# Optimization experiments

Measured on AMD Instinct MI355X. Metric: run time of the kernel, lower is better.

Reference implementation:

```python
import jax, jax.numpy as jnp
import numpy as np

B, CQ, CVK, L, H = 4, 256, 256, 2048, 8
D = CVK // H  # depth per head = 32
EPS = 1e-5    # BatchNorm eps


def setup_inputs() -> dict:
    key = jax.random.key(0)
    ks = jax.random.split(key, 32)
    n = lambda i, s, sc=1.0: jax.random.normal(ks[i], s, dtype=jnp.float32) * sc
    u = lambda i, s: jax.random.uniform(ks[i], s, dtype=jnp.float32, minval=0.5, maxval=1.5)
    inp = {
        'v': n(0, (B, CVK, L)), 'k': n(1, (B, CVK, L)), 'q': n(2, (B, CQ, L)),
        # trainable positional encodings (pe_q: image_shape_q, pe_vk: image_shape_vk)
        'pe_q': n(3, (CQ, L)), 'pe_vk': n(4, (CVK, L)),
        # W_query / W_key / W_value: Conv1d(kernel=1) weight [out,in] + bias, then BatchNorm1d (eval mode)
        'wq': n(5, (CVK, CQ), 0.05), 'bq': n(6, (CVK,), 0.05),
        'gq': 1.0 + n(7, (CVK,), 0.1), 'betaq': n(8, (CVK,), 0.1), 'mq': n(9, (CVK,), 0.1), 'varq': u(10, (CVK,)),
        'wk': n(11, (CVK, CVK), 0.05), 'bk': n(12, (CVK,), 0.05),
        'gk': 1.0 + n(13, (CVK,), 0.1), 'betak': n(14, (CVK,), 0.1), 'mk': n(15, (CVK,), 0.1), 'vark': u(16, (CVK,)),
        'wv': n(17, (CVK, CVK), 0.05), 'bv': n(18, (CVK,), 0.05),
        'gv': 1.0 + n(19, (CVK,), 0.1), 'betav': n(20, (CVK,), 0.1), 'mv': n(21, (CVK,), 0.1), 'varv': u(22, (CVK,)),
        # out_proj (zero-init in original; randomized here so gradients are non-trivial)
        'wo': n(23, (CQ, CVK), 0.05), 'bo': n(24, (CQ,), 0.05),
    }
    return inp


def _conv1(x, w, b):  # 1x1 conv == channel matmul: [b,c,l] -> [b,o,l]
    return jnp.einsum('oc,bcl->bol', w, x) + b[None, :, None]


def _bn(x, g, beta, mean, var):  # eval-mode BatchNorm1d over channel dim
    scale = g / jnp.sqrt(var + EPS)
    return (x - mean[:, None]) * scale[:, None] + beta[:, None]


def _mha(v, k, q, pe_q, pe_vk, wq, bq, gq, betaq, mq, varq,
         wk, bk, gk, betak, mk, vark, wv, bv, gv, betav, mv, varv, wo, bo):
    q_orig = q
    b = q.shape[0]
    vv = v + pe_vk[None]
    kk = k + pe_vk[None]
    qq = q + pe_q[None]
    qp = _bn(_conv1(qq, wq, bq), gq, betaq, mq, varq)   # [b, CVK, L]
    kp = _bn(_conv1(kk, wk, bk), gk, betak, mk, vark)
    vp = _bn(_conv1(vv, wv, bv), gv, betav, mv, varv)
    # split heads: [b, H, D, L]
    qh = qp.reshape(b, H, D, -1)
    kh = kp.reshape(b, H, D, -1)
    vh = vp.reshape(b, H, D, -1)
    # scaled dot-product attention over sequence dim (l: query pos, m: key pos)
    scores = jnp.einsum('bhdl,bhdm->bhlm', qh, kh) / jnp.sqrt(jnp.float32(D))
    p = jax.nn.softmax(scores, axis=-1)
    a = jnp.einsum('bhlm,bhdm->bhdl', p, vh)            # [b, H, D, L]
    a = a.reshape(b, H * D, -1)                          # [b, CVK, L]
    out = _conv1(a, wo, bo)                              # [b, CQ, L]
    return q_orig + out


def reference(v, k, q, pe_q, pe_vk, wq, bq, gq, betaq, mq, varq,
              wk, bk, gk, betak, mk, vark, wv, bv, gv, betav, mv, varv, wo, bo):
    return _mha(v, k, q, pe_q, pe_vk, wq, bq, gq, betaq, mq, varq,
                wk, bk, gk, betak, mk, vark, wv, bv, gv, betav, mv, varv, wo, bo)
```

## Files before the change

kernel.cpp:

```cpp
#include <hip/hip_runtime.h>
#include <hip/hip_bf16.h>

#define BB 4
#define CC 256
#define LL 2048
#define HH 8
#define DD 32
#define EPSV 1e-5f

typedef __bf16 bf16x8 __attribute__((ext_vector_type(8)));
typedef __bf16 bf16x4 __attribute__((ext_vector_type(4)));
typedef __bf16 bf16x2 __attribute__((ext_vector_type(2)));
typedef float  f32x4  __attribute__((ext_vector_type(4)));
typedef float  f32x16 __attribute__((ext_vector_type(16)));
typedef unsigned int u32x4 __attribute__((ext_vector_type(4)));

static __device__ __forceinline__ unsigned pkbf(float lo, float hi) {
    bf16x2 p; p[0] = (__bf16)lo; p[1] = (__bf16)hi;
    return __builtin_bit_cast(unsigned, p);
}

__global__ __launch_bounds__(512) void qkv_gemm_kernel(
    const float* __restrict__ qin, const float* __restrict__ kin,
    const float* __restrict__ vin,
    const float* __restrict__ peq, const float* __restrict__ pevk,
    const float* __restrict__ wq, const float* __restrict__ bq,
    const float* __restrict__ gq, const float* __restrict__ betaq,
    const float* __restrict__ mq, const float* __restrict__ varq,
    const float* __restrict__ wk, const float* __restrict__ bk,
    const float* __restrict__ gk, const float* __restrict__ betak,
    const float* __restrict__ mk, const float* __restrict__ vark,
    const float* __restrict__ wv, const float* __restrict__ bv,
    const float* __restrict__ gv, const float* __restrict__ betav,
    const float* __restrict__ mv, const float* __restrict__ varv,
    __bf16* __restrict__ qTo, __bf16* __restrict__ kTo, __bf16* __restrict__ vNo,
    float qscale)
{
    __shared__ __align__(16) __bf16 Wl[64][136];
    __shared__ __align__(16) __bf16 Xl[128][136];
    __bf16 (*Tl)[72] = (__bf16(*)[72])Xl;

    const int z = blockIdx.z;
    const int which = z >> 2;
    const int b = z & 3;
    const float* X    = which==0 ? qin : (which==1 ? kin : vin);
    const float* pe   = which==0 ? peq : pevk;
    const float* W    = which==0 ? wq  : (which==1 ? wk  : wv);
    const float* bia  = which==0 ? bq  : (which==1 ? bk  : bv);
    const float* gam  = which==0 ? gq  : (which==1 ? gk  : gv);
    const float* bet  = which==0 ? betaq : (which==1 ? betak : betav);
    const float* mea  = which==0 ? mq  : (which==1 ? mk  : mv);
    const float* var  = which==0 ? varq : (which==1 ? vark : varv);
    const float extra = (which==0) ? qscale : 1.0f;

    const int lt = blockIdx.x * 128;
    const int ot = blockIdx.y * 64;
    const int t  = threadIdx.x;
    const int wvi = t >> 6;
    const int wm = wvi >> 2;
    const int wn = wvi & 3;
    const int l  = t & 63;
    const int lq = l & 15;
    const int g  = l >> 4;

    f32x4 acc[2][2];
    #pragma unroll
    for (int mi = 0; mi < 2; ++mi)
        #pragma unroll
        for (int ni = 0; ni < 2; ++ni) acc[mi][ni] = (f32x4){0.f,0.f,0.f,0.f};

    for (int ks = 0; ks < 2; ++ks) {
        __syncthreads();
        #pragma unroll
        for (int i = 0; i < 4; ++i) {
            const int idx = i * 512 + t;
            const int row = idx >> 5;
            const int ch  = idx & 31;
            const int o   = ot + row;
            const float sc = gam[o] * rsqrtf(var[o] + EPSV) * extra;
            const float4 w4 = *(const float4*)&W[(size_t)o * CC + ks * 128 + ch * 4];
            bf16x4 wb;
            wb[0] = (__bf16)(w4.x * sc); wb[1] = (__bf16)(w4.y * sc);
            wb[2] = (__bf16)(w4.z * sc); wb[3] = (__bf16)(w4.w * sc);
            *(bf16x4*)&Wl[row][ch * 4] = wb;
        }
        #pragma unroll
        for (int i = 0; i < 2; ++i) {
            const int slot = i * 512 + t;
            const int lp = slot & 63;
            const int co = slot >> 6;
            const float* xp = &X[(size_t)(b * CC + ks * 128 + co * 8) * LL + lt + lp * 2];
            const float* pp = &pe[(size_t)(ks * 128 + co * 8) * LL + lt + lp * 2];
            bf16x8 lo, hi;
            #pragma unroll
            for (int j = 0; j < 8; ++j) {
                const float2 a = *(const float2*)&xp[(size_t)j * LL];
                const float2 p = *(const float2*)&pp[(size_t)j * LL];
                lo[j] = (__bf16)(a.x + p.x);
                hi[j] = (__bf16)(a.y + p.y);
            }
            *(bf16x8*)&Xl[lp * 2    ][co * 8] = lo;
            *(bf16x8*)&Xl[lp * 2 + 1][co * 8] = hi;
        }
        __syncthreads();

        #pragma unroll
        for (int kk = 0; kk < 4; ++kk) {
            bf16x8 af[2], bfr[2];
            #pragma unroll
            for (int mi = 0; mi < 2; ++mi)
                af[mi] = *(const bf16x8*)&Wl[wm * 32 + mi * 16 + lq][kk * 32 + g * 8];
            #pragma unroll
            for (int ni = 0; ni < 2; ++ni)
                bfr[ni] = *(const bf16x8*)&Xl[wn * 32 + ni * 16 + lq][kk * 32 + g * 8];
            #pragma unroll
            for (int mi = 0; mi < 2; ++mi)
                #pragma unroll
                for (int ni = 0; ni < 2; ++ni)
                    acc[mi][ni] = __builtin_amdgcn_mfma_f32_16x16x32_bf16(
                        af[mi], bfr[ni], acc[mi][ni], 0, 0, 0);
        }
    }

    float bb[2][4];
    #pragma unroll
    for (int mi = 0; mi < 2; ++mi) {
        const int o4 = ot + wm * 32 + mi * 16 + g * 4;
        const float4 b4 = *(const float4*)&bia[o4];
        const float4 g4 = *(const float4*)&gam[o4];
        const float4 v4 = *(const float4*)&var[o4];
        const float4 m4 = *(const float4*)&mea[o4];
        const float4 t4 = *(const float4*)&bet[o4];
        const float bs[4] = {b4.x,b4.y,b4.z,b4.w};
        const float gs[4] = {g4.x,g4.y,g4.z,g4.w};
        const float vs[4] = {v4.x,v4.y,v4.z,v4.w};
        const float ms[4] = {m4.x,m4.y,m4.z,m4.w};
        const float ts[4] = {t4.x,t4.y,t4.z,t4.w};
        #pragma unroll
        for (int r = 0; r < 4; ++r) {
            const float sc = gs[r] * rsqrtf(vs[r] + EPSV);
            bb[mi][r] = ((bs[r] - ms[r]) * sc + ts[r]) * extra;
        }
    }

    if (which < 2) {
        __bf16* outT = which==0 ? qTo : kTo;
        __syncthreads();
        #pragma unroll
        for (int mi = 0; mi < 2; ++mi) {
            #pragma unroll
            for (int ni = 0; ni < 2; ++ni) {
                bf16x4 pv;
                #pragma unroll
                for (int r = 0; r < 4; ++r) pv[r] = (__bf16)(acc[mi][ni][r] + bb[mi][r]);
                *(bf16x4*)&Tl[wn * 32 + ni * 16 + lq][wm * 32 + mi * 16 + g * 4] = pv;
            }
        }
        __syncthreads();
        #pragma unroll
        for (int i = 0; i < 2; ++i) {
            const int idx = i * 512 + t;
            const int lrow = idx >> 3, ch = idx & 7;
            *(bf16x8*)&outT[(size_t)(b * LL + lt + lrow) * CC + ot + ch * 8] =
                *(const bf16x8*)&Tl[lrow][ch * 8];
        }
    } else {
        #pragma unroll
        for (int mi = 0; mi < 2; ++mi) {
            #pragma unroll
            for (int ni = 0; ni < 2; ++ni) {
                const int col = lt + wn * 32 + ni * 16 + lq;
                #pragma unroll
                for (int r = 0; r < 4; ++r) {
                    const int o = ot + wm * 32 + mi * 16 + g * 4 + r;
                    vNo[(size_t)(b * CC + o) * LL + col] = (__bf16)(acc[mi][ni][r] + bb[mi][r]);
                }
            }
        }
    }
}

__global__ __launch_bounds__(256, 2) void attn_mfma_kernel(
    const __bf16* __restrict__ qT, const __bf16* __restrict__ kT,
    const __bf16* __restrict__ vN, __bf16* __restrict__ aT)
{
    __shared__ __align__(16) __bf16 KB[2][128 * 32];
    __shared__ __align__(16) __bf16 VB[2][32 * 128];

    const int flat = blockIdx.x + 16 * (blockIdx.y + 8 * blockIdx.z);
    const int xcd  = flat & 7;
    const int ixc  = flat >> 3;
    const int gidx = xcd + 8 * (ixc >> 4);
    const int qb   = ixc & 15;
    const int h    = gidx & 7;
    const int b    = gidx >> 3;

    const int t  = threadIdx.x;
    const int w  = t >> 6;
    const int l  = t & 63;
    const int lq = l & 31;
    const int hi = l >> 5;

    const int q0 = qb * 128 + w * 32;

    const __bf16* qrow = qT + ((size_t)(b * LL) + q0 + lq) * CC + h * DD;
    const bf16x8 qf0 = *(const bf16x8*)&qrow[hi * 8];
    const bf16x8 qf1 = *(const bf16x8*)&qrow[16 + hi * 8];

    const __bf16* kTb = kT + (size_t)(b * LL) * CC + h * DD;
    const __bf16* vNb = vN + ((size_t)(b * CC) + h * DD) * LL;

    const int s0 = t, s1 = 256 + t;
    const int sk0 = s0 >> 2, sp0 = s0 & 3;
    const int sk1 = s1 >> 2, sp1 = s1 & 3;
    const int sd0 = s0 >> 4, sv0 = s0 & 15;
    const int sd1 = s1 >> 4, sv1 = s1 & 15;
    const int kw0 = sk0 * 32 + (sp0 ^ ((sk0 >> 1) & 3)) * 8;
    const int kw1 = sk1 * 32 + (sp1 ^ ((sk1 >> 1) & 3)) * 8;
    const int vw0 = sd0 * 128 + (sv0 ^ (sd0 & 7)) * 8;
    const int vw1 = sd1 * 128 + (sv1 ^ (sd1 & 7)) * 8;

    bf16x8 kr0, kr1, vr0, vr1;
    #define LOADREGS(KT0) \
        kr0 = *(const bf16x8*)&kTb[(size_t)((KT0) + sk0) * CC + sp0 * 8]; \
        kr1 = *(const bf16x8*)&kTb[(size_t)((KT0) + sk1) * CC + sp1 * 8]; \
        vr0 = *(const bf16x8*)&vNb[(size_t)sd0 * LL + (KT0) + sv0 * 8];   \
        vr1 = *(const bf16x8*)&vNb[(size_t)sd1 * LL + (KT0) + sv1 * 8];
    #define WRITEBUF(BUF) \
        *(bf16x8*)&KB[BUF][kw0] = kr0; *(bf16x8*)&KB[BUF][kw1] = kr1; \
        *(bf16x8*)&VB[BUF][vw0] = vr0; *(bf16x8*)&VB[BUF][vw1] = vr1;

    LOADREGS(0)
    WRITEBUF(0)
    LOADREGS(128)

    f32x16 O;
    #pragma unroll
    for (int r = 0; r < 16; ++r) O[r] = 0.f;
    float ssum = 0.f;
    f32x16 Z16;
    #pragma unroll
    for (int r = 0; r < 16; ++r) Z16[r] = 0.f;

    #define QKC(kbv, S) { \
        const int key_ = (kbv) + lq; \
        const int ksw_ = (key_ >> 1) & 3; \
        const bf16x8 kf0_ = *(const bf16x8*)&KBb[key_ * 32 + ((hi    ) ^ ksw_) * 8]; \
        const bf16x8 kf1_ = *(const bf16x8*)&KBb[key_ * 32 + ((2 + hi) ^ ksw_) * 8]; \
        S = __builtin_amdgcn_mfma_f32_32x32x16_bf16(kf0_, qf0, Z16, 0, 0, 0); \
        S = __builtin_amdgcn_mfma_f32_32x32x16_bf16(kf1_, qf1, S, 0, 0, 0); }

    #define SMC(S, P0, P1) { \
        float e_[16]; \
        _Pragma("unroll") \
        for (int r = 0; r < 16; ++r) e_[r] = __builtin_amdgcn_exp2f(S[r]); \
        float s_ = 0.f; \
        _Pragma("unroll") \
        for (int r = 0; r < 16; r += 4) s_ += (e_[r] + e_[r+1]) + (e_[r+2] + e_[r+3]); \
        ssum += s_; \
        unsigned a_[8]; \
        _Pragma("unroll") \
        for (int i = 0; i < 8; ++i) a_[i] = pkbf(e_[2*i], e_[2*i+1]); \
        { unsigned w0_ = a_[0], w1_ = a_[1], w2_ = a_[2], w3_ = a_[3]; \
          asm volatile("v_permlane32_swap_b32 %0, %1" : "+v"(w0_), "+v"(w2_)); \
          asm volatile("v_permlane32_swap_b32 %0, %1" : "+v"(w1_), "+v"(w3_)); \
          P0 = (u32x4){w0_, w1_, w2_, w3_}; } \
        { unsigned w0_ = a_[4], w1_ = a_[5], w2_ = a_[6], w3_ = a_[7]; \
          asm volatile("v_permlane32_swap_b32 %0, %1" : "+v"(w0_), "+v"(w2_)); \
          asm volatile("v_permlane32_swap_b32 %0, %1" : "+v"(w1_), "+v"(w3_)); \
          P1 = (u32x4){w0_, w1_, w2_, w3_}; } }

    #define PVC(kbv, P0, P1) { \
        const bf16x8 pf0_ = __builtin_bit_cast(bf16x8, P0); \
        const bf16x8 vf0_ = *(const bf16x8*)&VBb[lq * 128 + ((((kbv) >> 3) + hi    ) ^ (lq & 7)) * 8]; \
        O = __builtin_amdgcn_mfma_f32_32x32x16_bf16(vf0_, pf0_, O, 0, 0, 0); \
        const bf16x8 pf1_ = __builtin_bit_cast(bf16x8, P1); \
        const bf16x8 vf1_ = *(const bf16x8*)&VBb[lq * 128 + ((((kbv) >> 3) + 2 + hi) ^ (lq & 7)) * 8]; \
        O = __builtin_amdgcn_mfma_f32_32x32x16_bf16(vf1_, pf1_, O, 0, 0, 0); }

    const int NT = LL / 128;
    for (int it = 0; it < NT; ++it) {
        const int buf = it & 1;
        __syncthreads();
        if (it + 1 < NT) { WRITEBUF(buf ^ 1) }
        if (it + 2 < NT) { LOADREGS((it + 2) * 128) }

        const __bf16* KBb = KB[buf];
        const __bf16* VBb = VB[buf];

        f32x16 S0, S1, S2, S3;
        u32x4 P0a, P0b, P1a, P1b, P2a, P2b, P3a, P3b;
        QKC(0,  S0)
        QKC(32, S1)
        SMC(S0, P0a, P0b)
        QKC(64, S2)
        PVC(0,  P0a, P0b)
        SMC(S1, P1a, P1b)
        QKC(96, S3)
        PVC(32, P1a, P1b)
        SMC(S2, P2a, P2b)
        PVC(64, P2a, P2b)
        SMC(S3, P3a, P3b)
        PVC(96, P3a, P3b)
    }
    #undef LOADREGS
    #undef WRITEBUF
    #undef QKC
    #undef SMC
    #undef PVC

    ssum += __shfl_xor(ssum, 32);
    const float inv = 1.f / ssum;

    __bf16* arow = aT + ((size_t)(b * LL) + q0 + lq) * CC + h * DD;
    #pragma unroll
    for (int gi = 0; gi < 4; ++gi) {
        bf16x4 ov;
        #pragma unroll
        for (int r = 0; r < 4; ++r) ov[r] = (__bf16)(O[4*gi + r] * inv);
        *(bf16x4*)&arow[8 * gi + 4 * hi] = ov;
    }
}

__global__ __launch_bounds__(256) void outproj_kernel(
    const float* __restrict__ W, const __bf16* __restrict__ X,
    const float* __restrict__ bias, const float* __restrict__ resid,
    float* __restrict__ outF)
{
    __shared__ __align__(16) __bf16 Wl[64][136];
    __shared__ __align__(16) __bf16 Xl[64][136];

    const int lt = blockIdx.x * 64;
    const int ot = blockIdx.y * 64;
    const int b  = blockIdx.z;
    const int t  = threadIdx.x;
    const int wvi = t >> 6;
    const int wm = wvi >> 1;
    const int wn = wvi & 1;
    const int l  = t & 63;
    const int lq = l & 15;
    const int g  = l >> 4;

    f32x4 acc[2][2];
    #pragma unroll
    for (int mi = 0; mi < 2; ++mi)
        #pragma unroll
        for (int ni = 0; ni < 2; ++ni) acc[mi][ni] = (f32x4){0.f,0.f,0.f,0.f};

    for (int ks = 0; ks < 2; ++ks) {
        __syncthreads();
        #pragma unroll
        for (int i = 0; i < 8; ++i) {
            const int idx = i * 256 + t;
            const int row = idx >> 5;
            const int ch  = idx & 31;
            const float4 w4 = *(const float4*)&W[(size_t)(ot + row) * CC + ks * 128 + ch * 4];
            bf16x4 wb;
            wb[0] = (__bf16)w4.x; wb[1] = (__bf16)w4.y;
            wb[2] = (__bf16)w4.z; wb[3] = (__bf16)w4.w;
            *(bf16x4*)&Wl[row][ch * 4] = wb;
        }
        #pragma unroll
        for (int i = 0; i < 4; ++i) {
            const int idx = i * 256 + t;
            const int row = idx >> 4, ch = idx & 15;
            *(bf16x8*)&Xl[row][ch * 8] =
                *(const bf16x8*)&X[(size_t)(b * LL + lt + row) * CC + ks * 128 + ch * 8];
        }
        __syncthreads();

        #pragma unroll
        for (int kk = 0; kk < 4; ++kk) {
            bf16x8 af[2], bfr[2];
            #pragma unroll
            for (int mi = 0; mi < 2; ++mi)
                af[mi] = *(const bf16x8*)&Wl[wm * 32 + mi * 16 + lq][kk * 32 + g * 8];
            #pragma unroll
            for (int ni = 0; ni < 2; ++ni)
                bfr[ni] = *(const bf16x8*)&Xl[wn * 32 + ni * 16 + lq][kk * 32 + g * 8];
            #pragma unroll
            for (int mi = 0; mi < 2; ++mi)
                #pragma unroll
                for (int ni = 0; ni < 2; ++ni)
                    acc[mi][ni] = __builtin_amdgcn_mfma_f32_16x16x32_bf16(
                        af[mi], bfr[ni], acc[mi][ni], 0, 0, 0);
        }
    }

    #pragma unroll
    for (int mi = 0; mi < 2; ++mi) {
        const float4 b4 = *(const float4*)&bias[ot + wm * 32 + mi * 16 + g * 4];
        const float bb[4] = {b4.x, b4.y, b4.z, b4.w};
        #pragma unroll
        for (int ni = 0; ni < 2; ++ni) {
            const int col = lt + wn * 32 + ni * 16 + lq;
            #pragma unroll
            for (int r = 0; r < 4; ++r) {
                const int o = ot + wm * 32 + mi * 16 + g * 4 + r;
                const size_t a = (size_t)(b * CC + o) * LL + col;
                outF[a] = acc[mi][ni][r] + bb[r] + resid[a];
            }
        }
    }
}

extern "C" void kernel_launch(void* const* d_in, const int* in_sizes, int n_in,
                              void* d_out, int out_size, void* d_ws, size_t ws_size,
                              hipStream_t stream)
{
    const float* v     = (const float*)d_in[0];
    const float* k     = (const float*)d_in[1];
    const float* q     = (const float*)d_in[2];
    const float* pe_q  = (const float*)d_in[3];
    const float* pe_vk = (const float*)d_in[4];
    const float* wq    = (const float*)d_in[5];
    const float* bq    = (const float*)d_in[6];
    const float* gq    = (const float*)d_in[7];
    const float* betaq = (const float*)d_in[8];
    const float* mq    = (const float*)d_in[9];
    const float* varq  = (const float*)d_in[10];
    const float* wk    = (const float*)d_in[11];
    const float* bk    = (const float*)d_in[12];
    const float* gk    = (const float*)d_in[13];
    const float* betak = (const float*)d_in[14];
    const float* mk    = (const float*)d_in[15];
    const float* vark  = (const float*)d_in[16];
    const float* wv    = (const float*)d_in[17];
    const float* bv    = (const float*)d_in[18];
    const float* gv    = (const float*)d_in[19];
    const float* betav = (const float*)d_in[20];
    const float* mv    = (const float*)d_in[21];
    const float* varv  = (const float*)d_in[22];
    const float* wo    = (const float*)d_in[23];
    const float* bo    = (const float*)d_in[24];

    float* out = (float*)d_out;

    const size_t E = (size_t)BB * CC * LL;
    __bf16* qT  = (__bf16*)d_ws;
    __bf16* kT  = qT + E;
    __bf16* vN  = kT + E;
    __bf16* aT  = vN + E;

    const float qscale = 0.17677669529663687f * 1.4426950408889634f;

    hipLaunchKernelGGL(qkv_gemm_kernel, dim3(16, 4, 12), dim3(512), 0, stream,
                       q, k, v, pe_q, pe_vk,
                       wq, bq, gq, betaq, mq, varq,
                       wk, bk, gk, betak, mk, vark,
                       wv, bv, gv, betav, mv, varv,
                       qT, kT, vN, qscale);

    hipLaunchKernelGGL(attn_mfma_kernel, dim3(16, HH, BB), dim3(256), 0, stream,
                       qT, kT, vN, aT);

    hipLaunchKernelGGL(outproj_kernel, dim3(32, 4, 4), dim3(256), 0, stream,
                       wo, aT, bo, q, out);
}
```

Measured before the change: 60.53 us.

## Split attention key range in two halves and add combine kernel

Attention blocks now each process half of the key sequence (split-K), doubling the grid from 512 to 1024 blocks. Each block writes unnormalized fp32 partial outputs and row sums to workspace, and a new combine kernel adds the two halves, normalizes and writes the bf16 attention output. The softmax has no running max, so the partials can simply be summed. The QK/PV schedule is also reordered to use fewer score registers, and the occupancy hint is dropped. This adds an extra launch and fp32 partial traffic (strided, uncoalesced-ish writes) in exchange for more parallelism.

```diff
diff --git a/kernel.cpp b/kernel.cpp
--- a/kernel.cpp
+++ b/kernel.cpp
@@ -180,20 +180,23 @@
     }
 }
 
-__global__ __launch_bounds__(256, 2) void attn_mfma_kernel(
+__global__ __launch_bounds__(256) void attn_mfma_kernel(
     const __bf16* __restrict__ qT, const __bf16* __restrict__ kT,
-    const __bf16* __restrict__ vN, __bf16* __restrict__ aT)
+    const __bf16* __restrict__ vN, float* __restrict__ Ow,
+    float* __restrict__ Sw)
 {
     __shared__ __align__(16) __bf16 KB[2][128 * 32];
     __shared__ __align__(16) __bf16 VB[2][32 * 128];
 
-    const int flat = blockIdx.x + 16 * (blockIdx.y + 8 * blockIdx.z);
+    const int flat = blockIdx.x + 16 * (blockIdx.y + 16 * blockIdx.z);
     const int xcd  = flat & 7;
     const int ixc  = flat >> 3;
     const int gidx = xcd + 8 * (ixc >> 4);
     const int qb   = ixc & 15;
-    const int h    = gidx & 7;
-    const int b    = gidx >> 3;
+    const int b    = gidx >> 4;
+    const int y    = gidx & 15;
+    const int h    = y >> 1;
+    const int half = y & 1;
 
     const int t  = threadIdx.x;
     const int w  = t >> 6;
@@ -202,6 +205,7 @@
     const int hi = l >> 5;
 
     const int q0 = qb * 128 + w * 32;
+    const int kbase = half * 1024;
 
     const __bf16* qrow = qT + ((size_t)(b * LL) + q0 + lq) * CC + h * DD;
     const bf16x8 qf0 = *(const bf16x8*)&qrow[hi * 8];
@@ -230,9 +234,9 @@
         *(bf16x8*)&KB[BUF][kw0] = kr0; *(bf16x8*)&KB[BUF][kw1] = kr1; \
         *(bf16x8*)&VB[BUF][vw0] = vr0; *(bf16x8*)&VB[BUF][vw1] = vr1;
 
-    LOADREGS(0)
+    LOADREGS(kbase)
     WRITEBUF(0)
-    LOADREGS(128)
+    LOADREGS(kbase + 128)
 
     f32x16 O;
     #pragma unroll
@@ -278,30 +282,30 @@
         const bf16x8 vf1_ = *(const bf16x8*)&VBb[lq * 128 + ((((kbv) >> 3) + 2 + hi) ^ (lq & 7)) * 8]; \
         O = __builtin_amdgcn_mfma_f32_32x32x16_bf16(vf1_, pf1_, O, 0, 0, 0); }
 
-    const int NT = LL / 128;
+    const int NT = 1024 / 128;
     for (int it = 0; it < NT; ++it) {
         const int buf = it & 1;
         __syncthreads();
         if (it + 1 < NT) { WRITEBUF(buf ^ 1) }
-        if (it + 2 < NT) { LOADREGS((it + 2) * 128) }
+        if (it + 2 < NT) { LOADREGS(kbase + (it + 2) * 128) }
 
         const __bf16* KBb = KB[buf];
         const __bf16* VBb = VB[buf];
 
-        f32x16 S0, S1, S2, S3;
-        u32x4 P0a, P0b, P1a, P1b, P2a, P2b, P3a, P3b;
+        f32x16 S0, S1;
+        u32x4 Pa, Pb;
         QKC(0,  S0)
         QKC(32, S1)
-        SMC(S0, P0a, P0b)
-        QKC(64, S2)
-        PVC(0,  P0a, P0b)
-        SMC(S1, P1a, P1b)
-        QKC(96, S3)
-        PVC(32, P1a, P1b)
-        SMC(S2, P2a, P2b)
-        PVC(64, P2a, P2b)
-        SMC(S3, P3a, P3b)
-        PVC(96, P3a, P3b)
+        SMC(S0, Pa, Pb)
+        PVC(0,  Pa, Pb)
+        QKC(64, S0)
+        SMC(S1, Pa, Pb)
+        PVC(32, Pa, Pb)
+        QKC(96, S1)
+        SMC(S0, Pa, Pb)
+        PVC(64, Pa, Pb)
+        SMC(S1, Pa, Pb)
+        PVC(96, Pa, Pb)
     }
     #undef LOADREGS
     #undef WRITEBUF
@@ -310,16 +314,53 @@
     #undef PVC
 
     ssum += __shfl_xor(ssum, 32);
-    const float inv = 1.f / ssum;
-
-    __bf16* arow = aT + ((size_t)(b * LL) + q0 + lq) * CC + h * DD;
+
+    float* orow = Ow + (size_t)(((b * HH + h) * 2 + half) * DD) * LL;
     #pragma unroll
     for (int gi = 0; gi < 4; ++gi) {
-        bf16x4 ov;
-        #pragma unroll
-        for (int r = 0; r < 4; ++r) ov[r] = (__bf16)(O[4*gi + r] * inv);
-        *(bf16x4*)&arow[8 * gi + 4 * hi] = ov;
-    }
+        #pragma unroll
+        for (int r = 0; r < 4; ++r) {
+            const int d = 8 * gi + 4 * hi + r;
+            orow[(size_t)d * LL + q0 + lq] = O[4 * gi + r];
+        }
+    }
+    if (l < 32)
+        Sw[(size_t)((b * HH + h) * 2 + half) * LL + q0 + lq] = ssum;
+}
+
+__global__ __launch_bounds__(256) void combine_kernel(
+    const float* __restrict__ Ow, const float* __restrict__ Sw,
+    __bf16* __restrict__ aT)
+{
+    __shared__ float invs[64];
+    __shared__ __align__(16) __bf16 Tl[64][40];
+
+    const int lt = blockIdx.x * 64;
+    const int h  = blockIdx.y;
+    const int b  = blockIdx.z;
+    const int t  = threadIdx.x;
+
+    if (t < 64) {
+        const float s0 = Sw[(size_t)((b * HH + h) * 2 + 0) * LL + lt + t];
+        const float s1 = Sw[(size_t)((b * HH + h) * 2 + 1) * LL + lt + t];
+        invs[t] = 1.f / (s0 + s1);
+    }
+    __syncthreads();
+
+    const float* O0 = Ow + (size_t)(((b * HH + h) * 2 + 0) * DD) * LL;
+    const float* O1 = Ow + (size_t)(((b * HH + h) * 2 + 1) * DD) * LL;
+    #pragma unroll
+    for (int i = 0; i < 8; ++i) {
+        const int idx = i * 256 + t;
+        const int d = idx >> 6, q = idx & 63;
+        const float v = (O0[(size_t)d * LL + lt + q] + O1[(size_t)d * LL + lt + q]) * invs[q];
+        Tl[q][d] = (__bf16)v;
+    }
+    __syncthreads();
+
+    const int q = t >> 2, dc = t & 3;
+    *(bf16x8*)&aT[((size_t)(b * LL) + lt + q) * CC + h * DD + dc * 8] =
+        *(const bf16x8*)&Tl[q][dc * 8];
 }
 
 __global__ __launch_bounds__(256) void outproj_kernel(
@@ -441,6 +482,8 @@
     __bf16* kT  = qT + E;
     __bf16* vN  = kT + E;
     __bf16* aT  = vN + E;
+    float*  Ow  = (float*)(aT + E);
+    float*  Sw  = Ow + 2 * E;
 
     const float qscale = 0.17677669529663687f * 1.4426950408889634f;
 
@@ -451,8 +494,11 @@
                        wv, bv, gv, betav, mv, varv,
                        qT, kT, vN, qscale);
 
-    hipLaunchKernelGGL(attn_mfma_kernel, dim3(16, HH, BB), dim3(256), 0, stream,
-                       qT, kT, vN, aT);
+    hipLaunchKernelGGL(attn_mfma_kernel, dim3(16, 16, BB), dim3(256), 0, stream,
+                       qT, kT, vN, Ow, Sw);
+
+    hipLaunchKernelGGL(combine_kernel, dim3(32, HH, BB), dim3(256), 0, stream,
+                       Ow, Sw, aT);
 
     hipLaunchKernelGGL(outproj_kernel, dim3(32, 4, 4), dim3(256), 0, stream,
                        wo, aT, bo, q, out);
```

Result: slower. 70.50 us (+16.5%).

## Split attention key range across two wave groups per block and merge via LDS

Applied to the files above, without the earlier changes.

The attention block doubles to 512 threads. Two halves each process half of the key sequence (1024 keys) with their own double-buffered K/V LDS tiles, and the partial O and row sums are combined through shared memory at the end. This is meant to raise parallelism and latency hiding given only 512 blocks on the GPU. The inner loop also reuses fewer S/P registers to reduce pressure. The merge only adds the partial sums with no max rescaling, so it is correct only if the softmax is computed without a running max. The extra LDS, barriers and combine step add cost.

```diff
diff --git a/kernel.cpp b/kernel.cpp
--- a/kernel.cpp
+++ b/kernel.cpp
@@ -180,12 +180,12 @@
     }
 }
 
-__global__ __launch_bounds__(256, 2) void attn_mfma_kernel(
+__global__ __launch_bounds__(512) void attn_mfma_kernel(
     const __bf16* __restrict__ qT, const __bf16* __restrict__ kT,
     const __bf16* __restrict__ vN, __bf16* __restrict__ aT)
 {
-    __shared__ __align__(16) __bf16 KB[2][128 * 32];
-    __shared__ __align__(16) __bf16 VB[2][32 * 128];
+    __shared__ __align__(16) __bf16 KB[2][2][4096];
+    __shared__ __align__(16) __bf16 VB[2][2][4096];
 
     const int flat = blockIdx.x + 16 * (blockIdx.y + 8 * blockIdx.z);
     const int xcd  = flat & 7;
@@ -197,11 +197,14 @@
 
     const int t  = threadIdx.x;
     const int w  = t >> 6;
+    const int hs = w >> 2;
+    const int wl = w & 3;
     const int l  = t & 63;
     const int lq = l & 31;
     const int hi = l >> 5;
 
-    const int q0 = qb * 128 + w * 32;
+    const int q0 = qb * 128 + wl * 32;
+    const int kbase = hs * 1024;
 
     const __bf16* qrow = qT + ((size_t)(b * LL) + q0 + lq) * CC + h * DD;
     const bf16x8 qf0 = *(const bf16x8*)&qrow[hi * 8];
@@ -210,7 +213,8 @@
     const __bf16* kTb = kT + (size_t)(b * LL) * CC + h * DD;
     const __bf16* vNb = vN + ((size_t)(b * CC) + h * DD) * LL;
 
-    const int s0 = t, s1 = 256 + t;
+    const int th = t & 255;
+    const int s0 = th, s1 = 256 + th;
     const int sk0 = s0 >> 2, sp0 = s0 & 3;
     const int sk1 = s1 >> 2, sp1 = s1 & 3;
     const int sd0 = s0 >> 4, sv0 = s0 & 15;
@@ -220,6 +224,9 @@
     const int vw0 = sd0 * 128 + (sv0 ^ (sd0 & 7)) * 8;
     const int vw1 = sd1 * 128 + (sv1 ^ (sd1 & 7)) * 8;
 
+    __bf16* KBw = &KB[hs][0][0];
+    __bf16* VBw = &VB[hs][0][0];
+
     bf16x8 kr0, kr1, vr0, vr1;
     #define LOADREGS(KT0) \
         kr0 = *(const bf16x8*)&kTb[(size_t)((KT0) + sk0) * CC + sp0 * 8]; \
@@ -227,12 +234,14 @@
         vr0 = *(const bf16x8*)&vNb[(size_t)sd0 * LL + (KT0) + sv0 * 8];   \
         vr1 = *(const bf16x8*)&vNb[(size_t)sd1 * LL + (KT0) + sv1 * 8];
     #define WRITEBUF(BUF) \
-        *(bf16x8*)&KB[BUF][kw0] = kr0; *(bf16x8*)&KB[BUF][kw1] = kr1; \
-        *(bf16x8*)&VB[BUF][vw0] = vr0; *(bf16x8*)&VB[BUF][vw1] = vr1;
-
-    LOADREGS(0)
+        *(bf16x8*)&KBw[(BUF) * 4096 + kw0] = kr0; \
+        *(bf16x8*)&KBw[(BUF) * 4096 + kw1] = kr1; \
+        *(bf16x8*)&VBw[(BUF) * 4096 + vw0] = vr0; \
+        *(bf16x8*)&VBw[(BUF) * 4096 + vw1] = vr1;
+
+    LOADREGS(kbase)
     WRITEBUF(0)
-    LOADREGS(128)
+    LOADREGS(kbase + 128)
 
     f32x16 O;
     #pragma unroll
@@ -278,30 +287,30 @@
         const bf16x8 vf1_ = *(const bf16x8*)&VBb[lq * 128 + ((((kbv) >> 3) + 2 + hi) ^ (lq & 7)) * 8]; \
         O = __builtin_amdgcn_mfma_f32_32x32x16_bf16(vf1_, pf1_, O, 0, 0, 0); }
 
-    const int NT = LL / 128;
+    const int NT = 1024 / 128;
     for (int it = 0; it < NT; ++it) {
         const int buf = it & 1;
         __syncthreads();
         if (it + 1 < NT) { WRITEBUF(buf ^ 1) }
-        if (it + 2 < NT) { LOADREGS((it + 2) * 128) }
-
-        const __bf16* KBb = KB[buf];
-        const __bf16* VBb = VB[buf];
-
-        f32x16 S0, S1, S2, S3;
-        u32x4 P0a, P0b, P1a, P1b, P2a, P2b, P3a, P3b;
+        if (it + 2 < NT) { LOADREGS(kbase + (it + 2) * 128) }
+
+        const __bf16* KBb = &KBw[buf * 4096];
+        const __bf16* VBb = &VBw[buf * 4096];
+
+        f32x16 S0, S1;
+        u32x4 Pa, Pb;
         QKC(0,  S0)
         QKC(32, S1)
-        SMC(S0, P0a, P0b)
-        QKC(64, S2)
-        PVC(0,  P0a, P0b)
-        SMC(S1, P1a, P1b)
-        QKC(96, S3)
-        PVC(32, P1a, P1b)
-        SMC(S2, P2a, P2b)
-        PVC(64, P2a, P2b)
-        SMC(S3, P3a, P3b)
-        PVC(96, P3a, P3b)
+        SMC(S0, Pa, Pb)
+        PVC(0,  Pa, Pb)
+        QKC(64, S0)
+        SMC(S1, Pa, Pb)
+        PVC(32, Pa, Pb)
+        QKC(96, S1)
+        SMC(S0, Pa, Pb)
+        PVC(64, Pa, Pb)
+        SMC(S1, Pa, Pb)
+        PVC(96, Pa, Pb)
     }
     #undef LOADREGS
     #undef WRITEBUF
@@ -310,15 +319,32 @@
     #undef PVC
 
     ssum += __shfl_xor(ssum, 32);
-    const float inv = 1.f / ssum;
-
-    __bf16* arow = aT + ((size_t)(b * LL) + q0 + lq) * CC + h * DD;
-    #pragma unroll
-    for (int gi = 0; gi < 4; ++gi) {
-        bf16x4 ov;
-        #pragma unroll
-        for (int r = 0; r < 4; ++r) ov[r] = (__bf16)(O[4*gi + r] * inv);
-        *(bf16x4*)&arow[8 * gi + 4 * hi] = ov;
+
+    __syncthreads();
+    float* Of = (float*)&KB[0][0][0];
+    float* Sf = (float*)&VB[0][0][0];
+
+    const int qloc = wl * 32 + lq;
+    if (hs == 1) {
+        #pragma unroll
+        for (int gi = 0; gi < 4; ++gi)
+            #pragma unroll
+            for (int r = 0; r < 4; ++r)
+                Of[qloc * 33 + 8 * gi + 4 * hi + r] = O[4 * gi + r];
+        if (l < 32) Sf[qloc] = ssum;
+    }
+    __syncthreads();
+    if (hs == 0) {
+        const float inv = 1.f / (ssum + Sf[qloc]);
+        __bf16* arow = aT + ((size_t)(b * LL) + q0 + lq) * CC + h * DD;
+        #pragma unroll
+        for (int gi = 0; gi < 4; ++gi) {
+            bf16x4 ov;
+            #pragma unroll
+            for (int r = 0; r < 4; ++r)
+                ov[r] = (__bf16)((O[4*gi + r] + Of[qloc * 33 + 8 * gi + 4 * hi + r]) * inv);
+            *(bf16x4*)&arow[8 * gi + 4 * hi] = ov;
+        }
     }
 }
 
@@ -451,7 +477,7 @@
                        wv, bv, gv, betav, mv, varv,
                        qT, kT, vN, qscale);
 
-    hipLaunchKernelGGL(attn_mfma_kernel, dim3(16, HH, BB), dim3(256), 0, stream,
+    hipLaunchKernelGGL(attn_mfma_kernel, dim3(16, HH, BB), dim3(512), 0, stream,
                        qT, kT, vN, aT);
 
     hipLaunchKernelGGL(outproj_kernel, dim3(32, 4, 4), dim3(256), 0, stream,
```

Result: no change. 61.18 us (+1.1%).
